# Optimization experiments

Measured on AMD Instinct MI355X. Metric: run time of the kernel, lower is better.

The kernel has to match this reference:

```python
import jax, jax.numpy as jnp
import numpy as np

N = 100000      # total nodes in batched graph
E = 1600000     # edges (avg degree 16)
G = 128         # graphs in batch
K = 3           # Chebyshev order
LAMBDA_MAX = 2.0  # standard bound for normalized Laplacian


def setup_inputs() -> dict:
    key = jax.random.key(0)
    ks = jax.random.split(key, 24)
    d = {}
    d["signal"] = jax.random.normal(ks[0], (N, 128), dtype=jnp.float32)
    # ChebConv linears: Linear(k*in, out) per DGL
    dims = [(K * 128, 128), (K * 128, 128), (K * 128, 256), (K * 256, 512)]
    for i, (fi, fo) in enumerate(dims):
        d[f"W{i}"] = jax.random.normal(ks[1 + 2 * i], (fi, fo), dtype=jnp.float32) * (1.0 / np.sqrt(fi))
        d[f"b{i}"] = jnp.zeros((fo,), dtype=jnp.float32)
    d["Wm1"] = jax.random.normal(ks[10], (512, 512), dtype=jnp.float32) * (1.0 / np.sqrt(512))
    d["bm1"] = jnp.zeros((512,), dtype=jnp.float32)
    d["Wm2"] = jax.random.normal(ks[11], (512, 10), dtype=jnp.float32) * (1.0 / np.sqrt(512))
    d["bm2"] = jnp.zeros((10,), dtype=jnp.float32)
    d["src"] = jax.random.randint(ks[12], (E,), 0, N)
    d["dst"] = jax.random.randint(ks[13], (E,), 0, N)
    d["graph_ids"] = jnp.sort(jax.random.randint(ks[14], (N,), 0, G))
    return d


def _cheb_conv(x, W, b, src, dst, norm, re_norm):
    # Ahat = D^-1/2 A D^-1/2 applied via gather/scatter over edges
    def ahat(h):
        return norm * jax.ops.segment_sum((h * norm)[src], dst, num_segments=N)

    X0 = x
    terms = [X0]
    X1 = -re_norm * ahat(X0) + (re_norm - 1.0) * X0
    terms.append(X1)
    Xpp, Xp = X0, X1
    for _ in range(2, K):
        Xi = -2.0 * re_norm * ahat(Xp) + 2.0 * (re_norm - 1.0) * Xp - Xpp
        terms.append(Xi)
        Xpp, Xp = Xp, Xi
    h = jnp.concatenate(terms, axis=1) @ W + b
    return jax.nn.relu(h)  # DGL ChebConv default activation


def reference(signal, W0, b0, W1, b1, W2, b2, W3, b3, Wm1, bm1, Wm2, bm2,
              src, dst, graph_ids):
    deg = jax.ops.segment_sum(jnp.ones((E,), dtype=signal.dtype), dst, num_segments=N)
    norm = jnp.clip(deg, 1.0, None) ** -0.5  # [N]
    norm = norm[:, None]
    re_norm = 2.0 / LAMBDA_MAX

    h = signal
    for W, b in ((W0, b0), (W1, b1), (W2, b2), (W3, b3)):
        h = _cheb_conv(h, W, b, src, dst, norm, re_norm)

    # readout='sum': per-graph sum over nodes -> [G, 512]
    hg = jax.ops.segment_sum(h, graph_ids, num_segments=G)

    # MLP classifier
    return jax.nn.relu(hg @ Wm1 + bm1) @ Wm2 + bm2
```

## Files before the change

### kernel.cpp

```cpp
#include <hip/hip_runtime.h>
#include <hip/hip_bf16.h>

#define N_NODES 100000
#define PAD_N   100096
#define N_EDGES 1600000
#define N_GRAPH 128
#define SCAN_B  1024
#define SCAN_G  ((N_NODES + SCAN_B - 1) / SCAN_B)

typedef unsigned short u16;
typedef __attribute__((ext_vector_type(4))) float f32x4;
typedef __attribute__((ext_vector_type(8))) short s16x8;

__device__ __forceinline__ float bf2f(u16 u) {
  unsigned int v = ((unsigned int)u) << 16;
  float f; __builtin_memcpy(&f, &v, 4); return f;
}
__device__ __forceinline__ u16 f2bf(float f) {
  unsigned int v; __builtin_memcpy(&v, &f, 4);
  return (u16)((v + 0x7FFFu + ((v >> 16) & 1u)) >> 16);
}
__device__ __forceinline__ void glds16(const u16* g, u16* l) {
  __builtin_amdgcn_global_load_lds(
      (const __attribute__((address_space(1))) unsigned int*)g,
      (__attribute__((address_space(3))) unsigned int*)l, 16, 0, 0);
}

__global__ void k_deg(const int* __restrict__ dst, int* __restrict__ degi) {
  int e = blockIdx.x * 256 + threadIdx.x;
  if (e < N_EDGES) atomicAdd(&degi[dst[e]], 1);
}

__global__ void k_norm(const int* __restrict__ degi, float* __restrict__ nrm) {
  int i = blockIdx.x * 256 + threadIdx.x;
  if (i < N_NODES) {
    int d = degi[i]; if (d < 1) d = 1;
    nrm[i] = 1.0f / sqrtf((float)d);
  }
}

__global__ void k_scan1(const int* __restrict__ degi, int* __restrict__ rowptr,
                        int* __restrict__ bsum) {
  __shared__ int sm[SCAN_B];
  int i = blockIdx.x * SCAN_B + threadIdx.x;
  int v = (i < N_NODES) ? degi[i] : 0;
  sm[threadIdx.x] = v;
  __syncthreads();
  for (int off = 1; off < SCAN_B; off <<= 1) {
    int t = (threadIdx.x >= off) ? sm[threadIdx.x - off] : 0;
    __syncthreads();
    sm[threadIdx.x] += t;
    __syncthreads();
  }
  if (i < N_NODES) rowptr[i] = sm[threadIdx.x] - v;
  if (threadIdx.x == SCAN_B - 1) bsum[blockIdx.x] = sm[SCAN_B - 1];
}

__global__ void k_scan2(const int* __restrict__ bsum, int* __restrict__ boff,
                        int* __restrict__ rowptr) {
  __shared__ int sm[128];
  int v = (threadIdx.x < SCAN_G) ? bsum[threadIdx.x] : 0;
  sm[threadIdx.x] = v;
  __syncthreads();
  for (int off = 1; off < 128; off <<= 1) {
    int t = (threadIdx.x >= off) ? sm[threadIdx.x - off] : 0;
    __syncthreads();
    sm[threadIdx.x] += t;
    __syncthreads();
  }
  if (threadIdx.x < SCAN_G) boff[threadIdx.x] = sm[threadIdx.x] - v;
  if (threadIdx.x == 127) rowptr[N_NODES] = sm[127];
}

__global__ void k_scan3(int* __restrict__ rowptr, const int* __restrict__ boff) {
  int i = blockIdx.x * SCAN_B + threadIdx.x;
  if (i < N_NODES) rowptr[i] += boff[blockIdx.x];
}

__global__ void k_scatter(const int* __restrict__ src, const int* __restrict__ dst,
                          const int* __restrict__ rowptr, int* __restrict__ cursor,
                          int* __restrict__ colidx) {
  int e = blockIdx.x * 256 + threadIdx.x;
  if (e >= N_EDGES) return;
  int d = dst[e];
  int p = atomicAdd(&cursor[d], 1);
  colidx[rowptr[d] + p] = src[e];
}

__global__ void k_wsplit(const float* __restrict__ W, u16* __restrict__ th,
                         int F, int fout) {
  int K3 = 3 * F;
  int i = blockIdx.x * 256 + threadIdx.x;
  if (i >= K3 * fout) return;
  int k = i / fout, n = i % fout;
  float v;
  if (k < F)          v = W[(size_t)k * fout + n] - W[(size_t)(k + 2 * F) * fout + n];
  else if (k < 2 * F) v = W[(size_t)k * fout + n];
  else                v = -2.0f * W[(size_t)k * fout + n];
  th[(size_t)n * K3 + k] = f2bf(v);
}

__global__ void k_sigcast(const float* __restrict__ s, u16* __restrict__ h) {
  int i = blockIdx.x * 256 + threadIdx.x;
  if (i >= PAD_N * 128) return;
  float v = (i < N_NODES * 128) ? s[i] : 0.f;
  h[i] = f2bf(v);
}

template<int VEC>
__global__ void k_ahat_bf(const u16* __restrict__ gh, const float* __restrict__ nrm,
                          const int* __restrict__ rowptr, const int* __restrict__ colidx,
                          u16* __restrict__ oh, int F, int base, int nrows, float alpha) {
  int nl = (blockIdx.x * blockDim.x + threadIdx.x) >> 6;
  int lane = threadIdx.x & 63;
  if (nl >= nrows) return;
  int node = base + nl;
  int fo = lane * VEC;
  float res[VEC];
  if (node < N_NODES) {
    float acc[VEC];
#pragma unroll
    for (int v = 0; v < VEC; ++v) acc[v] = 0.f;
    int e0 = __builtin_amdgcn_readfirstlane(rowptr[node]);
    int e1 = __builtin_amdgcn_readfirstlane(rowptr[node + 1]);
    int e = e0;
    for (; e + 8 <= e1; e += 8) {
      int ss[8]; float nn[8];
#pragma unroll
      for (int j = 0; j < 8; ++j) ss[j] = colidx[e + j];
#pragma unroll
      for (int j = 0; j < 8; ++j) nn[j] = nrm[ss[j]];
      if constexpr (VEC == 2) {
        unsigned int uu[8];
#pragma unroll
        for (int j = 0; j < 8; ++j) uu[j] = *(const unsigned int*)(gh + (size_t)ss[j] * F + fo);
#pragma unroll
        for (int j = 0; j < 8; ++j) {
          acc[0] += bf2f((u16)uu[j]) * nn[j];
          acc[1] += bf2f((u16)(uu[j] >> 16)) * nn[j];
        }
      } else {
        uint2 uu[8];
#pragma unroll
        for (int j = 0; j < 8; ++j) uu[j] = *(const uint2*)(gh + (size_t)ss[j] * F + fo);
#pragma unroll
        for (int j = 0; j < 8; ++j) {
          acc[0] += bf2f((u16)uu[j].x) * nn[j];
          acc[1] += bf2f((u16)(uu[j].x >> 16)) * nn[j];
          acc[2] += bf2f((u16)uu[j].y) * nn[j];
          acc[3] += bf2f((u16)(uu[j].y >> 16)) * nn[j];
        }
      }
    }
    for (; e + 4 <= e1; e += 4) {
      int ss[4]; float nn[4];
#pragma unroll
      for (int j = 0; j < 4; ++j) ss[j] = colidx[e + j];
#pragma unroll
      for (int j = 0; j < 4; ++j) nn[j] = nrm[ss[j]];
      if constexpr (VEC == 2) {
        unsigned int uu[4];
#pragma unroll
        for (int j = 0; j < 4; ++j) uu[j] = *(const unsigned int*)(gh + (size_t)ss[j] * F + fo);
#pragma unroll
        for (int j = 0; j < 4; ++j) {
          acc[0] += bf2f((u16)uu[j]) * nn[j];
          acc[1] += bf2f((u16)(uu[j] >> 16)) * nn[j];
        }
      } else {
        uint2 uu[4];
#pragma unroll
        for (int j = 0; j < 4; ++j) uu[j] = *(const uint2*)(gh + (size_t)ss[j] * F + fo);
#pragma unroll
        for (int j = 0; j < 4; ++j) {
          acc[0] += bf2f((u16)uu[j].x) * nn[j];
          acc[1] += bf2f((u16)(uu[j].x >> 16)) * nn[j];
          acc[2] += bf2f((u16)uu[j].y) * nn[j];
          acc[3] += bf2f((u16)(uu[j].y >> 16)) * nn[j];
        }
      }
    }
    for (; e < e1; ++e) {
      int s = colidx[e];
      float ns = nrm[s];
      const u16* ph = gh + (size_t)s * F + fo;
      if constexpr (VEC == 2) {
        unsigned int uh = *(const unsigned int*)ph;
        acc[0] += bf2f((u16)uh) * ns;
        acc[1] += bf2f((u16)(uh >> 16)) * ns;
      } else {
        uint2 uh = *(const uint2*)ph;
        acc[0] += bf2f((u16)uh.x) * ns;
        acc[1] += bf2f((u16)(uh.x >> 16)) * ns;
        acc[2] += bf2f((u16)uh.y) * ns;
        acc[3] += bf2f((u16)(uh.y >> 16)) * ns;
      }
    }
    float sc2 = alpha * nrm[node];
#pragma unroll
    for (int v = 0; v < VEC; ++v) res[v] = sc2 * acc[v];
  } else {
#pragma unroll
    for (int v = 0; v < VEC; ++v) res[v] = 0.f;
  }
  u16* po = oh + (size_t)nl * F + fo;
  if constexpr (VEC == 2) {
    *(unsigned int*)po = (unsigned int)f2bf(res[0]) | ((unsigned int)f2bf(res[1]) << 16);
  } else {
    uint2 w;
    w.x = (unsigned int)f2bf(res[0]) | ((unsigned int)f2bf(res[1]) << 16);
    w.y = (unsigned int)f2bf(res[2]) | ((unsigned int)f2bf(res[3]) << 16);
    *(uint2*)po = w;
  }
}


template<bool POOL>
__launch_bounds__(512, 4)
__global__ void k_gemm_mfma(const u16* __restrict__ A0, const u16* __restrict__ A1,
                            const u16* __restrict__ A2, int F,
                            const u16* __restrict__ Bth,
                            const float* __restrict__ bias, u16* __restrict__ O,
                            float* __restrict__ hg, const int* __restrict__ gid,
                            int fout, int nrows) {
  __shared__ u16 As[2][128][32];
  __shared__ u16 Bs[2][128][32];
  const int tid = threadIdx.x;
  const int lane = tid & 63, wid = tid >> 6;
  const int wm = wid >> 2, wn = wid & 3;
  const int row0 = blockIdx.y * 128, col0 = blockIdx.x * 128;
  const int K3 = 3 * F;
  const int li = lane & 15, kq = lane >> 4;
  const int sidx = tid >> 2;
  const int skg = (tid & 3) ^ ((sidx >> 1) & 3);
  const size_t dso = (size_t)wid * 512;
  const int slot = (kq ^ ((li >> 1) & 3)) * 8;

  auto stage = [&](int t, int b) {
    int k0 = t * 32;
    const u16* S; int kk;
    if (k0 < F)          { S = A0; kk = k0; }
    else if (k0 < 2 * F) { S = A1; kk = k0 - F; }
    else                 { S = A2; kk = k0 - 2 * F; }
    glds16(S + (size_t)(row0 + sidx) * F + (kk + skg * 8), &As[b][0][0] + dso);
    glds16(Bth + (size_t)(col0 + sidx) * K3 + (k0 + skg * 8), &Bs[b][0][0] + dso);
  };

  f32x4 acc[4][2];
#pragma unroll
  for (int m = 0; m < 4; ++m)
#pragma unroll
    for (int n = 0; n < 2; ++n) acc[m][n] = (f32x4){0.f, 0.f, 0.f, 0.f};

  const int NT = K3 / 32;
  stage(0, 0);
  stage(1, 1);
  for (int t = 0; t < NT; ++t) {
    if (t + 1 < NT) asm volatile("s_waitcnt vmcnt(2)" ::: "memory");
    else            asm volatile("s_waitcnt vmcnt(0)" ::: "memory");
    __builtin_amdgcn_sched_barrier(0);
    __builtin_amdgcn_s_barrier();
    const int cb = t & 1;
    s16x8 a[4], bh[2];
#pragma unroll
    for (int m = 0; m < 4; ++m)
      a[m] = *(const s16x8*)&As[cb][wm * 64 + m * 16 + li][slot];
#pragma unroll
    for (int n = 0; n < 2; ++n)
      bh[n] = *(const s16x8*)&Bs[cb][wn * 32 + n * 16 + li][slot];
    asm volatile("s_waitcnt lgkmcnt(0)" ::: "memory");
    __builtin_amdgcn_sched_barrier(0);
    __builtin_amdgcn_s_barrier();
    if (t + 2 < NT) stage(t + 2, cb);
    __builtin_amdgcn_s_setprio(1);
#pragma unroll
    for (int m = 0; m < 4; ++m)
#pragma unroll
      for (int n = 0; n < 2; ++n)
        acc[m][n] = __builtin_amdgcn_mfma_f32_16x16x32_bf16(a[m], bh[n], acc[m][n], 0, 0, 0);
    __builtin_amdgcn_s_setprio(0);
  }

  if (!POOL) {
#pragma unroll
    for (int m = 0; m < 4; ++m) {
      int rbase = row0 + wm * 64 + m * 16 + kq * 4;
#pragma unroll
      for (int n = 0; n < 2; ++n) {
        int col = col0 + wn * 32 + n * 16 + li;
        float bi = bias[col];
#pragma unroll
        for (int r2 = 0; r2 < 4; ++r2) {
          int rr = rbase + r2;
          if (rr < nrows)
            O[(size_t)rr * fout + col] = f2bf(fmaxf(acc[m][n][r2] + bi, 0.f));
        }
      }
    }
  } else {
#pragma unroll
    for (int m = 0; m < 4; ++m) {
      int rbase = row0 + wm * 64 + m * 16 + kq * 4;
      int g4[4];
#pragma unroll
      for (int r2 = 0; r2 < 4; ++r2) {
        int rr = rbase + r2;
        g4[r2] = (rr < nrows) ? gid[rr] : -1;
      }
#pragma unroll
      for (int n = 0; n < 2; ++n) {
        int col = col0 + wn * 32 + n * 16 + li;
        float bi = bias[col];
        float sum = 0.f; int curg = g4[0];
#pragma unroll
        for (int r2 = 0; r2 < 4; ++r2) {
          if (g4[r2] != curg) {
            if (curg >= 0) atomicAdd(&hg[curg * 512 + col], sum);
            sum = 0.f; curg = g4[r2];
          }
          if (g4[r2] >= 0) sum += fmaxf(acc[m][n][r2] + bi, 0.f);
        }
        if (curg >= 0) atomicAdd(&hg[curg * 512 + col], sum);
      }
    }
  }
}

template<bool POOL>
__launch_bounds__(512, 4)
__global__ void k_gemm_wide(const u16* __restrict__ A0, const u16* __restrict__ A1,
                            const u16* __restrict__ A2, int F,
                            const u16* __restrict__ Bth,
                            const float* __restrict__ bias, u16* __restrict__ O,
                            float* __restrict__ hg, const int* __restrict__ gid,
                            int fout, int nrows) {
  __shared__ u16 As[2][128][32];
  __shared__ u16 Bs[2][256][32];
  const int tid = threadIdx.x;
  const int lane = tid & 63, wid = tid >> 6;
  const int wm = wid >> 2, wn = wid & 3;
  const int row0 = blockIdx.y * 128, col0 = blockIdx.x * 256;
  const int K3 = 3 * F;
  const int li = lane & 15, kq = lane >> 4;
  const int sidx = tid >> 2;
  const int skg = (tid & 3) ^ ((sidx >> 1) & 3);
  const size_t dsoA = (size_t)wid * 512;
  const int slot = (kq ^ ((li >> 1) & 3)) * 8;

  auto stage = [&](int t, int b) {
    int k0 = t * 32;
    const u16* S; int kk;
    if (k0 < F)          { S = A0; kk = k0; }
    else if (k0 < 2 * F) { S = A1; kk = k0 - F; }
    else                 { S = A2; kk = k0 - 2 * F; }
    glds16(S + (size_t)(row0 + sidx) * F + (kk + skg * 8), &As[b][0][0] + dsoA);
#pragma unroll
    for (int r = 0; r < 2; ++r) {
      int s = r * 512 + tid;
      int col = s >> 2;
      int kgB = (s & 3) ^ ((col >> 1) & 3);
      glds16(Bth + (size_t)(col0 + col) * K3 + (k0 + kgB * 8),
             &Bs[b][0][0] + (size_t)(r * 512 + wid * 64) * 8);
    }
  };

  f32x4 acc[4][4];
#pragma unroll
  for (int m = 0; m < 4; ++m)
#pragma unroll
    for (int n = 0; n < 4; ++n) acc[m][n] = (f32x4){0.f, 0.f, 0.f, 0.f};

  const int NT = K3 / 32;
  stage(0, 0);
  stage(1, 1);
  for (int t = 0; t < NT; ++t) {
    if (t + 1 < NT) asm volatile("s_waitcnt vmcnt(3)" ::: "memory");
    else            asm volatile("s_waitcnt vmcnt(0)" ::: "memory");
    __builtin_amdgcn_sched_barrier(0);
    __builtin_amdgcn_s_barrier();
    const int cb = t & 1;
    s16x8 a[4], b[4];
#pragma unroll
    for (int m = 0; m < 4; ++m)
      a[m] = *(const s16x8*)&As[cb][wm * 64 + m * 16 + li][slot];
#pragma unroll
    for (int n = 0; n < 4; ++n)
      b[n] = *(const s16x8*)&Bs[cb][wn * 64 + n * 16 + li][slot];
    asm volatile("s_waitcnt lgkmcnt(0)" ::: "memory");
    __builtin_amdgcn_sched_barrier(0);
    __builtin_amdgcn_s_barrier();
    if (t + 2 < NT) stage(t + 2, cb);
    __builtin_amdgcn_s_setprio(1);
#pragma unroll
    for (int m = 0; m < 4; ++m)
#pragma unroll
      for (int n = 0; n < 4; ++n)
        acc[m][n] = __builtin_amdgcn_mfma_f32_16x16x32_bf16(a[m], b[n], acc[m][n], 0, 0, 0);
    __builtin_amdgcn_s_setprio(0);
  }

  if (!POOL) {
#pragma unroll
    for (int m = 0; m < 4; ++m) {
      int rbase = row0 + wm * 64 + m * 16 + kq * 4;
#pragma unroll
      for (int n = 0; n < 4; ++n) {
        int col = col0 + wn * 64 + n * 16 + li;
        float bi = bias[col];
#pragma unroll
        for (int r2 = 0; r2 < 4; ++r2) {
          int rr = rbase + r2;
          if (rr < nrows)
            O[(size_t)rr * fout + col] = f2bf(fmaxf(acc[m][n][r2] + bi, 0.f));
        }
      }
    }
  } else {
#pragma unroll
    for (int m = 0; m < 4; ++m) {
      int rbase = row0 + wm * 64 + m * 16 + kq * 4;
      int g4[4];
#pragma unroll
      for (int r2 = 0; r2 < 4; ++r2) {
        int rr = rbase + r2;
        g4[r2] = (rr < nrows) ? gid[rr] : -1;
      }
#pragma unroll
      for (int n = 0; n < 4; ++n) {
        int col = col0 + wn * 64 + n * 16 + li;
        float bi = bias[col];
        float sum = 0.f; int curg = g4[0];
#pragma unroll
        for (int r2 = 0; r2 < 4; ++r2) {
          if (g4[r2] != curg) {
            if (curg >= 0) atomicAdd(&hg[curg * 512 + col], sum);
            sum = 0.f; curg = g4[r2];
          }
          if (g4[r2] >= 0) sum += fmaxf(acc[m][n][r2] + bi, 0.f);
        }
        if (curg >= 0) atomicAdd(&hg[curg * 512 + col], sum);
      }
    }
  }
}

__global__ void k_mlp(const float* __restrict__ hg, const float* __restrict__ Wm1,
                      const float* __restrict__ bm1, const float* __restrict__ Wm2,
                      const float* __restrict__ bm2, float* __restrict__ outp) {
  __shared__ float lh[512];
  __shared__ float lt[512];
  int g = blockIdx.x, t = threadIdx.x;
  lh[t] = hg[g * 512 + t];
  __syncthreads();
  float s = bm1[t];
  for (int k = 0; k < 512; ++k) s += lh[k] * Wm1[k * 512 + t];
  lt[t] = fmaxf(s, 0.f);
  __syncthreads();
  if (t < 10) {
    float s2 = bm2[t];
    for (int j = 0; j < 512; ++j) s2 += lt[j] * Wm2[j * 10 + t];
    outp[g * 10 + t] = s2;
  }
}

extern "C" void kernel_launch(void* const* d_in, const int* in_sizes, int n_in,
                              void* d_out, int out_size, void* d_ws, size_t ws_size,
                              hipStream_t stream) {
  (void)in_sizes; (void)n_in; (void)out_size;
  const float* signal = (const float*)d_in[0];
  const float* W0 = (const float*)d_in[1];  const float* b0 = (const float*)d_in[2];
  const float* W1 = (const float*)d_in[3];  const float* b1 = (const float*)d_in[4];
  const float* W2 = (const float*)d_in[5];  const float* b2 = (const float*)d_in[6];
  const float* W3 = (const float*)d_in[7];  const float* b3 = (const float*)d_in[8];
  const float* Wm1 = (const float*)d_in[9];  const float* bm1 = (const float*)d_in[10];
  const float* Wm2 = (const float*)d_in[11]; const float* bm2 = (const float*)d_in[12];
  const int* src = (const int*)d_in[13];
  const int* dst = (const int*)d_in[14];
  const int* gid = (const int*)d_in[15];
  float* outp = (float*)d_out;

  char* ws = (char*)d_ws;
  size_t off = 0;
  auto alloc = [&](size_t b) -> void* {
    void* p = ws + off;
    off = (off + b + 255) & ~(size_t)255;
    return p;
  };
  int* degi    = (int*)alloc((size_t)N_NODES * 4);
  float* nrm   = (float*)alloc((size_t)N_NODES * 4);
  int* rowptr  = (int*)alloc((size_t)(N_NODES + 1) * 4);
  int* cursor  = (int*)alloc((size_t)N_NODES * 4);
  int* bsum    = (int*)alloc((size_t)SCAN_G * 4);
  int* boff    = (int*)alloc((size_t)SCAN_G * 4);
  int* colidx  = (int*)alloc((size_t)N_EDGES * 4);
  float* hg    = (float*)alloc((size_t)N_GRAPH * 512 * 4);
  u16* Wth0 = (u16*)alloc((size_t)384 * 128 * 2);
  u16* Wth1 = (u16*)alloc((size_t)384 * 128 * 2);
  u16* Wth2 = (u16*)alloc((size_t)384 * 256 * 2);
  u16* Wth3 = (u16*)alloc((size_t)768 * 512 * 2);
  u16* QA = (u16*)alloc((size_t)PAD_N * 256 * 2);
  u16* QB = (u16*)alloc((size_t)PAD_N * 128 * 2);
  u16* QX = (u16*)alloc((size_t)PAD_N * 256 * 2);
  const size_t yneed = (size_t)PAD_N * 256 * 2;
  u16* QY = nullptr;
  if (ws_size > off && ws_size - off >= yneed + 512) QY = (u16*)alloc(yneed);

  hipMemsetAsync(degi, 0, (size_t)N_NODES * 4, stream);
  hipMemsetAsync(cursor, 0, (size_t)N_NODES * 4, stream);
  hipMemsetAsync(hg, 0, (size_t)N_GRAPH * 512 * 4, stream);

  k_deg<<<(N_EDGES + 255) / 256, 256, 0, stream>>>(dst, degi);
  k_norm<<<(N_NODES + 255) / 256, 256, 0, stream>>>(degi, nrm);
  k_scan1<<<SCAN_G, SCAN_B, 0, stream>>>(degi, rowptr, bsum);
  k_scan2<<<1, 128, 0, stream>>>(bsum, boff, rowptr);
  k_scan3<<<SCAN_G, SCAN_B, 0, stream>>>(rowptr, boff);
  k_scatter<<<(N_EDGES + 255) / 256, 256, 0, stream>>>(src, dst, rowptr, cursor, colidx);

  k_wsplit<<<(384 * 128 + 255) / 256, 256, 0, stream>>>(W0, Wth0, 128, 128);
  k_wsplit<<<(384 * 128 + 255) / 256, 256, 0, stream>>>(W1, Wth1, 128, 128);
  k_wsplit<<<(384 * 256 + 255) / 256, 256, 0, stream>>>(W2, Wth2, 128, 256);
  k_wsplit<<<(768 * 512 + 255) / 256, 256, 0, stream>>>(W3, Wth3, 256, 512);
  k_sigcast<<<(PAD_N * 128 + 255) / 256, 256, 0, stream>>>(signal, QB);

  const int gfull = (PAD_N + 3) / 4;

  u16* X1h = QX;
  u16* Yh  = QX + (size_t)PAD_N * 128;
  auto layer128 = [&](const u16* in, const u16* wth, const float* bias, u16* outb) {
    k_ahat_bf<2><<<gfull, 256, 0, stream>>>(in,  nrm, rowptr, colidx, X1h, 128, 0, PAD_N, -1.f);
    k_ahat_bf<2><<<gfull, 256, 0, stream>>>(X1h, nrm, rowptr, colidx, Yh,  128, 0, PAD_N,  1.f);
    dim3 gg(1, PAD_N / 128);
    k_gemm_mfma<false><<<gg, 512, 0, stream>>>(in, X1h, Yh, 128, wth, bias,
                                               outb, nullptr, nullptr, 128, N_NODES);
  };
  layer128(QB, Wth0, b0, QA);
  layer128(QA, Wth1, b1, QB);

  k_ahat_bf<2><<<gfull, 256, 0, stream>>>(QB,  nrm, rowptr, colidx, X1h, 128, 0, PAD_N, -1.f);
  k_ahat_bf<2><<<gfull, 256, 0, stream>>>(X1h, nrm, rowptr, colidx, Yh,  128, 0, PAD_N,  1.f);
  {
    dim3 gg(1, PAD_N / 128);
    k_gemm_wide<false><<<gg, 512, 0, stream>>>(QB, X1h, Yh, 128, Wth2, b2,
                                               QA, nullptr, nullptr, 256, N_NODES);
  }

  k_ahat_bf<4><<<gfull, 256, 0, stream>>>(QA, nrm, rowptr, colidx, QX, 256, 0, PAD_N, -1.f);
  if (QY != nullptr) {
    k_ahat_bf<4><<<gfull, 256, 0, stream>>>(QX, nrm, rowptr, colidx, QY, 256, 0, PAD_N, 1.f);
    dim3 gg(2, PAD_N / 128);
    k_gemm_wide<true><<<gg, 512, 0, stream>>>(QA, QX, QY, 256, Wth3, b3,
                                              nullptr, hg, gid, 512, N_NODES);
  } else {
    const int CH4 = 50048;
    for (int base = 0; base < N_NODES; base += CH4) {
      int nr = (N_NODES - base < CH4) ? (N_NODES - base) : CH4;
      k_ahat_bf<4><<<(nr + 3) / 4, 256, 0, stream>>>(QX, nrm, rowptr, colidx, QB,
                                                     256, base, nr, 1.f);
      dim3 gg(4, (nr + 127) / 128);
      k_gemm_mfma<true><<<gg, 512, 0, stream>>>(
          QA + (size_t)base * 256, QX + (size_t)base * 256, QB, 256,
          Wth3, b3, nullptr, hg, gid + base, 512, nr);
    }
  }

  k_mlp<<<N_GRAPH, 512, 0, stream>>>(hg, Wm1, bm1, Wm2, bm2, outp);
}
```

Measured before the change: 1.157 ms.

## Use a 128x512 fat-tile GEMM for the final ChebConv layer

Adds a new MFMA GEMM kernel whose block computes a 128-row by full 512-column output tile, replacing the previous two-block-wide launch for the last layer. Each A tile (the three Chebyshev terms) is now loaded once per row block instead of once per column half, which halves A traffic. The kernel double-buffers LDS tiles, uses swizzled LDS slots, and keeps the fused bias/ReLU/segment-sum atomics epilogue. In exchange it uses 128 accumulator registers per thread and a large LDS footprint (about 80KB), which may limit occupancy, and it launches half as many blocks.

```diff
diff --git a/kernel.cpp b/kernel.cpp
--- a/kernel.cpp
+++ b/kernel.cpp
@@ -440,6 +440,105 @@
         }
         if (curg >= 0) atomicAdd(&hg[curg * 512 + col], sum);
       }
+    }
+  }
+}
+
+__launch_bounds__(512, 2)
+__global__ void k_gemm_fat(const u16* __restrict__ A0, const u16* __restrict__ A1,
+                           const u16* __restrict__ A2, int F,
+                           const u16* __restrict__ Bth,
+                           const float* __restrict__ bias,
+                           float* __restrict__ hg, const int* __restrict__ gid,
+                           int nrows) {
+  __shared__ u16 As[2][128][32];
+  __shared__ u16 Bs[2][512][32];
+  const int tid = threadIdx.x;
+  const int lane = tid & 63, wid = tid >> 6;
+  const int wm = wid >> 2, wn = wid & 3;
+  const int row0 = blockIdx.y * 128;
+  const int K3 = 3 * F;
+  const int li = lane & 15, kq = lane >> 4;
+  const int sidx = tid >> 2;
+  const int skg = (tid & 3) ^ ((sidx >> 1) & 3);
+  const size_t dsoA = (size_t)wid * 512;
+  const int slot = (kq ^ ((li >> 1) & 3)) * 8;
+
+  auto stage = [&](int t, int b) {
+    int k0 = t * 32;
+    const u16* S; int kk;
+    if (k0 < F)          { S = A0; kk = k0; }
+    else if (k0 < 2 * F) { S = A1; kk = k0 - F; }
+    else                 { S = A2; kk = k0 - 2 * F; }
+    glds16(S + (size_t)(row0 + sidx) * F + (kk + skg * 8), &As[b][0][0] + dsoA);
+#pragma unroll
+    for (int r = 0; r < 4; ++r) {
+      int s = r * 512 + tid;
+      int col = s >> 2;
+      int kgB = (s & 3) ^ ((col >> 1) & 3);
+      glds16(Bth + (size_t)col * K3 + (k0 + kgB * 8),
+             &Bs[b][0][0] + (size_t)(r * 512 + wid * 64) * 8);
+    }
+  };
+
+  f32x4 acc[4][8];
+#pragma unroll
+  for (int m = 0; m < 4; ++m)
+#pragma unroll
+    for (int n = 0; n < 8; ++n) acc[m][n] = (f32x4){0.f, 0.f, 0.f, 0.f};
+
+  const int NT = K3 / 32;
+  stage(0, 0);
+  stage(1, 1);
+  for (int t = 0; t < NT; ++t) {
+    if (t + 1 < NT) asm volatile("s_waitcnt vmcnt(5)" ::: "memory");
+    else            asm volatile("s_waitcnt vmcnt(0)" ::: "memory");
+    __builtin_amdgcn_sched_barrier(0);
+    __builtin_amdgcn_s_barrier();
+    const int cb = t & 1;
+    s16x8 a[4], b[8];
+#pragma unroll
+    for (int m = 0; m < 4; ++m)
+      a[m] = *(const s16x8*)&As[cb][wm * 64 + m * 16 + li][slot];
+#pragma unroll
+    for (int n = 0; n < 8; ++n)
+      b[n] = *(const s16x8*)&Bs[cb][wn * 128 + n * 16 + li][slot];
+    asm volatile("s_waitcnt lgkmcnt(0)" ::: "memory");
+    __builtin_amdgcn_sched_barrier(0);
+    __builtin_amdgcn_s_barrier();
+    if (t + 2 < NT) stage(t + 2, cb);
+    __builtin_amdgcn_s_setprio(1);
+#pragma unroll
+    for (int m = 0; m < 4; ++m)
+#pragma unroll
+      for (int n = 0; n < 8; ++n)
+        acc[m][n] = __builtin_amdgcn_mfma_f32_16x16x32_bf16(a[m], b[n], acc[m][n], 0, 0, 0);
+    __builtin_amdgcn_s_setprio(0);
+  }
+
+#pragma unroll
+  for (int m = 0; m < 4; ++m) {
+    int rbase = row0 + wm * 64 + m * 16 + kq * 4;
+    int g4[4];
+#pragma unroll
+    for (int r2 = 0; r2 < 4; ++r2) {
+      int rr = rbase + r2;
+      g4[r2] = (rr < nrows) ? gid[rr] : -1;
+    }
+#pragma unroll
+    for (int n = 0; n < 8; ++n) {
+      int col = wn * 128 + n * 16 + li;
+      float bi = bias[col];
+      float sum = 0.f; int curg = g4[0];
+#pragma unroll
+      for (int r2 = 0; r2 < 4; ++r2) {
+        if (g4[r2] != curg) {
+          if (curg >= 0) atomicAdd(&hg[curg * 512 + col], sum);
+          sum = 0.f; curg = g4[r2];
+        }
+        if (g4[r2] >= 0) sum += fmaxf(acc[m][n][r2] + bi, 0.f);
+      }
+      if (curg >= 0) atomicAdd(&hg[curg * 512 + col], sum);
     }
   }
 }
@@ -547,9 +646,8 @@
   k_ahat_bf<4><<<gfull, 256, 0, stream>>>(QA, nrm, rowptr, colidx, QX, 256, 0, PAD_N, -1.f);
   if (QY != nullptr) {
     k_ahat_bf<4><<<gfull, 256, 0, stream>>>(QX, nrm, rowptr, colidx, QY, 256, 0, PAD_N, 1.f);
-    dim3 gg(2, PAD_N / 128);
-    k_gemm_wide<true><<<gg, 512, 0, stream>>>(QA, QX, QY, 256, Wth3, b3,
-                                              nullptr, hg, gid, 512, N_NODES);
+    dim3 gg(1, PAD_N / 128);
+    k_gemm_fat<<<gg, 512, 0, stream>>>(QA, QX, QY, 256, Wth3, b3, hg, gid, N_NODES);
   } else {
     const int CH4 = 50048;
     for (int base = 0; base < N_NODES; base += CH4) {
```

Measured after the change: 1.173 ms. About the same (+1.4%).

## Replace wide GEMM with 256x256-tile eight-phase pipelined MFMA kernel

Applied to the files above, without the earlier changes.

The 128x256 wide GEMM used by the last two Chebyshev layers is replaced by a 256x256 output tile. Each 64-wide K step is split into half-steps, and the half-step loads for the next step are interleaved with LDS reads and MFMA bursts in an eight-phase schedule. The larger tile is meant to raise operand reuse from LDS and to hide global-to-LDS latency better. In exchange it doubles LDS and accumulator registers, cuts occupancy to 2 blocks per CU, and halves the grid, which may leave CUs idle when rows run out.

```diff
diff --git a/kernel.cpp b/kernel.cpp
--- a/kernel.cpp
+++ b/kernel.cpp
@@ -213,7 +213,6 @@
     *(uint2*)po = w;
   }
 }
-
 
 template<bool POOL>
 __launch_bounds__(512, 4)
@@ -327,82 +326,136 @@
 }
 
 template<bool POOL>
-__launch_bounds__(512, 4)
-__global__ void k_gemm_wide(const u16* __restrict__ A0, const u16* __restrict__ A1,
-                            const u16* __restrict__ A2, int F,
-                            const u16* __restrict__ Bth,
-                            const float* __restrict__ bias, u16* __restrict__ O,
-                            float* __restrict__ hg, const int* __restrict__ gid,
-                            int fout, int nrows) {
-  __shared__ u16 As[2][128][32];
-  __shared__ u16 Bs[2][256][32];
+__launch_bounds__(512, 2)
+__global__ void k_gemm_8ph(const u16* __restrict__ A0, const u16* __restrict__ A1,
+                           const u16* __restrict__ A2, int F,
+                           const u16* __restrict__ Bth,
+                           const float* __restrict__ bias, u16* __restrict__ O,
+                           float* __restrict__ hg, const int* __restrict__ gid,
+                           int fout, int nrows) {
+  __shared__ u16 As[2][2][256][32];
+  __shared__ u16 Bs[2][2][256][32];
   const int tid = threadIdx.x;
   const int lane = tid & 63, wid = tid >> 6;
   const int wm = wid >> 2, wn = wid & 3;
-  const int row0 = blockIdx.y * 128, col0 = blockIdx.x * 256;
+  const int row0 = blockIdx.y * 256, col0 = blockIdx.x * 256;
   const int K3 = 3 * F;
   const int li = lane & 15, kq = lane >> 4;
-  const int sidx = tid >> 2;
-  const int skg = (tid & 3) ^ ((sidx >> 1) & 3);
-  const size_t dsoA = (size_t)wid * 512;
   const int slot = (kq ^ ((li >> 1) & 3)) * 8;
-
-  auto stage = [&](int t, int b) {
-    int k0 = t * 32;
+  const int srow = wid * 16 + (lane >> 2);
+  const int squar = lane & 3;
+  const size_t sdst = (size_t)(wid * 16) * 32;
+
+  auto stageA = [&](int t, int kh, int b) {
+    int k0 = t * 64 + kh * 32;
     const u16* S; int kk;
     if (k0 < F)          { S = A0; kk = k0; }
     else if (k0 < 2 * F) { S = A1; kk = k0 - F; }
     else                 { S = A2; kk = k0 - 2 * F; }
-    glds16(S + (size_t)(row0 + sidx) * F + (kk + skg * 8), &As[b][0][0] + dsoA);
 #pragma unroll
     for (int r = 0; r < 2; ++r) {
-      int s = r * 512 + tid;
-      int col = s >> 2;
-      int kgB = (s & 3) ^ ((col >> 1) & 3);
-      glds16(Bth + (size_t)(col0 + col) * K3 + (k0 + kgB * 8),
-             &Bs[b][0][0] + (size_t)(r * 512 + wid * 64) * 8);
-    }
-  };
-
-  f32x4 acc[4][4];
-#pragma unroll
-  for (int m = 0; m < 4; ++m)
+      int row = r * 128 + srow;
+      int q = squar ^ ((row >> 1) & 3);
+      glds16(S + (size_t)(row0 + row) * F + (kk + q * 8),
+             &As[b][kh][0][0] + sdst + (size_t)r * 128 * 32);
+    }
+  };
+  auto stageB = [&](int t, int kh, int b) {
+    int k0 = t * 64 + kh * 32;
+#pragma unroll
+    for (int r = 0; r < 2; ++r) {
+      int col = r * 128 + srow;
+      int q = squar ^ ((col >> 1) & 3);
+      glds16(Bth + (size_t)(col0 + col) * K3 + (k0 + q * 8),
+             &Bs[b][kh][0][0] + sdst + (size_t)r * 128 * 32);
+    }
+  };
+
+  f32x4 acc[8][4];
+#pragma unroll
+  for (int m = 0; m < 8; ++m)
 #pragma unroll
     for (int n = 0; n < 4; ++n) acc[m][n] = (f32x4){0.f, 0.f, 0.f, 0.f};
 
-  const int NT = K3 / 32;
-  stage(0, 0);
-  stage(1, 1);
+  s16x8 a[4], bb[4];
+  auto readA = [&](int b, int kh, int mh) {
+#pragma unroll
+    for (int i = 0; i < 4; ++i)
+      a[i] = *(const s16x8*)&As[b][kh][wm * 128 + (mh * 4 + i) * 16 + li][slot];
+  };
+  auto readB = [&](int b, int kh) {
+#pragma unroll
+    for (int n = 0; n < 4; ++n)
+      bb[n] = *(const s16x8*)&Bs[b][kh][wn * 64 + n * 16 + li][slot];
+  };
+  auto mm0 = [&]() {
+    __builtin_amdgcn_s_setprio(1);
+#pragma unroll
+    for (int i = 0; i < 4; ++i)
+#pragma unroll
+      for (int n = 0; n < 4; ++n)
+        acc[i][n] = __builtin_amdgcn_mfma_f32_16x16x32_bf16(a[i], bb[n], acc[i][n], 0, 0, 0);
+    __builtin_amdgcn_s_setprio(0);
+  };
+  auto mm1 = [&]() {
+    __builtin_amdgcn_s_setprio(1);
+#pragma unroll
+    for (int i = 0; i < 4; ++i)
+#pragma unroll
+      for (int n = 0; n < 4; ++n)
+        acc[4 + i][n] = __builtin_amdgcn_mfma_f32_16x16x32_bf16(a[i], bb[n], acc[4 + i][n], 0, 0, 0);
+    __builtin_amdgcn_s_setprio(0);
+  };
+
+  const int NT = K3 / 64;
+  stageA(0, 0, 0); stageB(0, 0, 0); stageA(0, 1, 0); stageB(0, 1, 0);
+  asm volatile("s_waitcnt vmcnt(4)" ::: "memory");
+  __builtin_amdgcn_sched_barrier(0);
+  __builtin_amdgcn_s_barrier();
+
   for (int t = 0; t < NT; ++t) {
-    if (t + 1 < NT) asm volatile("s_waitcnt vmcnt(3)" ::: "memory");
-    else            asm volatile("s_waitcnt vmcnt(0)" ::: "memory");
-    __builtin_amdgcn_sched_barrier(0);
-    __builtin_amdgcn_s_barrier();
-    const int cb = t & 1;
-    s16x8 a[4], b[4];
-#pragma unroll
-    for (int m = 0; m < 4; ++m)
-      a[m] = *(const s16x8*)&As[cb][wm * 64 + m * 16 + li][slot];
-#pragma unroll
-    for (int n = 0; n < 4; ++n)
-      b[n] = *(const s16x8*)&Bs[cb][wn * 64 + n * 16 + li][slot];
+    const int cb = t & 1, nb = cb ^ 1;
+    const bool st = (t + 1 < NT);
+    readA(cb, 0, 0); readB(cb, 0);
+    if (st) stageA(t + 1, 0, nb);
+    __builtin_amdgcn_s_barrier();
     asm volatile("s_waitcnt lgkmcnt(0)" ::: "memory");
     __builtin_amdgcn_sched_barrier(0);
-    __builtin_amdgcn_s_barrier();
-    if (t + 2 < NT) stage(t + 2, cb);
-    __builtin_amdgcn_s_setprio(1);
-#pragma unroll
-    for (int m = 0; m < 4; ++m)
-#pragma unroll
-      for (int n = 0; n < 4; ++n)
-        acc[m][n] = __builtin_amdgcn_mfma_f32_16x16x32_bf16(a[m], b[n], acc[m][n], 0, 0, 0);
-    __builtin_amdgcn_s_setprio(0);
+    mm0();
+    __builtin_amdgcn_s_barrier();
+    readA(cb, 0, 1);
+    if (st) stageB(t + 1, 0, nb);
+    __builtin_amdgcn_s_barrier();
+    asm volatile("s_waitcnt lgkmcnt(0)" ::: "memory");
+    __builtin_amdgcn_sched_barrier(0);
+    mm1();
+    if (st) asm volatile("s_waitcnt vmcnt(4)" ::: "memory");
+    else    asm volatile("s_waitcnt vmcnt(0)" ::: "memory");
+    __builtin_amdgcn_sched_barrier(0);
+    __builtin_amdgcn_s_barrier();
+    readA(cb, 1, 0); readB(cb, 1);
+    if (st) stageA(t + 1, 1, nb);
+    __builtin_amdgcn_s_barrier();
+    asm volatile("s_waitcnt lgkmcnt(0)" ::: "memory");
+    __builtin_amdgcn_sched_barrier(0);
+    mm0();
+    __builtin_amdgcn_s_barrier();
+    readA(cb, 1, 1);
+    if (st) stageB(t + 1, 1, nb);
+    __builtin_amdgcn_s_barrier();
+    asm volatile("s_waitcnt lgkmcnt(0)" ::: "memory");
+    __builtin_amdgcn_sched_barrier(0);
+    mm1();
+    if (st) asm volatile("s_waitcnt vmcnt(4)" ::: "memory");
+    else    asm volatile("s_waitcnt vmcnt(0)" ::: "memory");
+    __builtin_amdgcn_sched_barrier(0);
+    __builtin_amdgcn_s_barrier();
   }
 
   if (!POOL) {
 #pragma unroll
-    for (int m = 0; m < 4; ++m) {
-      int rbase = row0 + wm * 64 + m * 16 + kq * 4;
+    for (int m = 0; m < 8; ++m) {
+      int rbase = row0 + wm * 128 + m * 16 + kq * 4;
 #pragma unroll
       for (int n = 0; n < 4; ++n) {
         int col = col0 + wn * 64 + n * 16 + li;
@@ -417,8 +470,8 @@
     }
   } else {
 #pragma unroll
-    for (int m = 0; m < 4; ++m) {
-      int rbase = row0 + wm * 64 + m * 16 + kq * 4;
+    for (int m = 0; m < 8; ++m) {
+      int rbase = row0 + wm * 128 + m * 16 + kq * 4;
       int g4[4];
 #pragma unroll
       for (int r2 = 0; r2 < 4; ++r2) {
@@ -539,17 +592,17 @@
   k_ahat_bf<2><<<gfull, 256, 0, stream>>>(QB,  nrm, rowptr, colidx, X1h, 128, 0, PAD_N, -1.f);
   k_ahat_bf<2><<<gfull, 256, 0, stream>>>(X1h, nrm, rowptr, colidx, Yh,  128, 0, PAD_N,  1.f);
   {
-    dim3 gg(1, PAD_N / 128);
-    k_gemm_wide<false><<<gg, 512, 0, stream>>>(QB, X1h, Yh, 128, Wth2, b2,
-                                               QA, nullptr, nullptr, 256, N_NODES);
+    dim3 gg(1, PAD_N / 256);
+    k_gemm_8ph<false><<<gg, 512, 0, stream>>>(QB, X1h, Yh, 128, Wth2, b2,
+                                              QA, nullptr, nullptr, 256, N_NODES);
   }
 
   k_ahat_bf<4><<<gfull, 256, 0, stream>>>(QA, nrm, rowptr, colidx, QX, 256, 0, PAD_N, -1.f);
   if (QY != nullptr) {
     k_ahat_bf<4><<<gfull, 256, 0, stream>>>(QX, nrm, rowptr, colidx, QY, 256, 0, PAD_N, 1.f);
-    dim3 gg(2, PAD_N / 128);
-    k_gemm_wide<true><<<gg, 512, 0, stream>>>(QA, QX, QY, 256, Wth3, b3,
-                                              nullptr, hg, gid, 512, N_NODES);
+    dim3 gg(2, PAD_N / 256);
+    k_gemm_8ph<true><<<gg, 512, 0, stream>>>(QA, QX, QY, 256, Wth3, b3,
+                                             nullptr, hg, gid, 512, N_NODES);
   } else {
     const int CH4 = 50048;
     for (int base = 0; base < N_NODES; base += CH4) {
```

Measured after the change: 1.206 ms. +4.3%, slower.
